# Optimization experiments

Hardware: AMD Instinct MI355X
Metric: run time of the kernel (lower is better)

Reference implementation:

```python
import jax, jax.numpy as jnp
import numpy as np

N_NODES = 50000


def _gcn_norm(edge_index, num_nodes):
    """Add self-loops and compute symmetric GCN normalization per edge.
    Returns (src, dst, norm) with src/dst of length E + N."""
    loop = jnp.arange(num_nodes, dtype=edge_index.dtype)
    src = jnp.concatenate([edge_index[0], loop])
    dst = jnp.concatenate([edge_index[1], loop])
    ones = jnp.ones(dst.shape[0], dtype=jnp.float32)
    deg = jax.ops.segment_sum(ones, dst, num_segments=num_nodes)
    dinv = jnp.where(deg > 0, jax.lax.rsqrt(deg), 0.0)
    norm = dinv[src] * dinv[dst]  # [E + N]
    return src, dst, norm


def _gcn_conv(x, src, dst, norm, W, b, num_nodes):
    h = x @ W                                # [N, out]
    msg = h[src] * norm[:, None]             # gather + scale, [E+N, out]
    out = jax.ops.segment_sum(msg, dst, num_segments=num_nodes)  # scatter-add
    return out + b


def setup_inputs() -> dict:
    key = jax.random.key(0)
    ks = jax.random.split(key, 10)
    F, H = 128, 128
    x = jax.random.normal(ks[0], (N_NODES, F), dtype=jnp.float32)
    edge_index = jax.random.randint(ks[1], (2, 800000), 0, N_NODES, dtype=jnp.int64)
    def glorot(k, fan_in, fan_out):
        s = (6.0 / (fan_in + fan_out)) ** 0.5
        return jax.random.uniform(k, (fan_in, fan_out), jnp.float32, -s, s)
    return {
        "x": x,
        "edge_index": edge_index,
        "W1": glorot(ks[2], F, H), "b1": jnp.zeros((H,), jnp.float32),
        "W2": glorot(ks[3], H, H), "b2": jnp.zeros((H,), jnp.float32),
        "W3": glorot(ks[4], H, H), "b3": jnp.zeros((H,), jnp.float32),
        "W4": glorot(ks[5], H, F), "b4": jnp.zeros((F,), jnp.float32),
    }


def reference(x, edge_index, W1, b1, W2, b2, W3, b3, W4, b4):
    n = x.shape[0]
    src, dst, norm = _gcn_norm(edge_index, n)  # same edges for all 4 layers
    h = jax.nn.relu(_gcn_conv(x, src, dst, norm, W1, b1, n))
    h = jax.nn.relu(_gcn_conv(h, src, dst, norm, W2, b2, n))
    h = jax.nn.relu(_gcn_conv(h, src, dst, norm, W3, b3, n))
    h = jax.nn.relu(_gcn_conv(h, src, dst, norm, W4, b4, n))
    return h
```

## Files before the change

### kernel.cpp

```cpp
#include <hip/hip_runtime.h>
#include <hip/hip_fp16.h>

typedef __attribute__((ext_vector_type(8))) _Float16 half8;
typedef __attribute__((ext_vector_type(4))) float f32x4;

static __device__ __forceinline__ half8 as_half8(uint4 u) {
    union { uint4 u; half8 h; } c; c.u = u; return c.h;
}


__global__ void prep_k(int* __restrict__ cnt, const float* __restrict__ x,
                       __half* __restrict__ Xh, int N) {
    int stride = gridDim.x * 256;
    int tid = blockIdx.x * 256 + threadIdx.x;
    for (int i = tid; i < 12544; i += stride) ((int4*)cnt)[i] = make_int4(0, 0, 0, 0);
    int nOut = N * 16;
    const float4* x4 = (const float4*)x;
    uint4* o4 = (uint4*)Xh;
    for (int i = tid; i < nOut; i += stride) {
        float4 f0 = x4[i * 2 + 0];
        float4 f1 = x4[i * 2 + 1];
        __half2 h0 = __floats2half2_rn(f0.x, f0.y);
        __half2 h1 = __floats2half2_rn(f0.z, f0.w);
        __half2 h2 = __floats2half2_rn(f1.x, f1.y);
        __half2 h3 = __floats2half2_rn(f1.z, f1.w);
        uint4 o;
        o.x = *(unsigned int*)&h0;
        o.y = *(unsigned int*)&h1;
        o.z = *(unsigned int*)&h2;
        o.w = *(unsigned int*)&h3;
        o4[i] = o;
    }
}

__global__ void hist_rank_k(const int* __restrict__ dst, int* __restrict__ cnt,
                            int* __restrict__ rank, int E) {
    int e4 = blockIdx.x * 256 + threadIdx.x;
    int nE4 = E >> 2;
    if (e4 < nE4) {
        int4 d = ((const int4*)dst)[e4];
        int4 r;
        r.x = atomicAdd(&cnt[d.x], 1);
        r.y = atomicAdd(&cnt[d.y], 1);
        r.z = atomicAdd(&cnt[d.z], 1);
        r.w = atomicAdd(&cnt[d.w], 1);
        ((int4*)rank)[e4] = r;
    } else if (e4 == nE4) {
        for (int e = nE4 * 4; e < E; ++e) rank[e] = atomicAdd(&cnt[dst[e]], 1);
    }
}

__global__ void bsum_k(const int* __restrict__ cnt, int* __restrict__ bsum,
                       float* __restrict__ dinv, int n) {
    int b = blockIdx.x, tid = threadIdx.x;
    int base = b * 1024 + tid * 4;
    int4 v = make_int4(0, 0, 0, 0);
    if (base + 3 < n) v = *(const int4*)(cnt + base);
    else {
        if (base + 0 < n) v.x = cnt[base + 0];
        if (base + 1 < n) v.y = cnt[base + 1];
        if (base + 2 < n) v.z = cnt[base + 2];
    }
    if (base + 3 < n) {
        float4 dv;
        dv.x = rsqrtf((float)v.x + 1.0f);
        dv.y = rsqrtf((float)v.y + 1.0f);
        dv.z = rsqrtf((float)v.z + 1.0f);
        dv.w = rsqrtf((float)v.w + 1.0f);
        *(float4*)(dinv + base) = dv;
    } else {
        if (base + 0 < n) dinv[base + 0] = rsqrtf((float)v.x + 1.0f);
        if (base + 1 < n) dinv[base + 1] = rsqrtf((float)v.y + 1.0f);
        if (base + 2 < n) dinv[base + 2] = rsqrtf((float)v.z + 1.0f);
    }
    int s = v.x + v.y + v.z + v.w;
#pragma unroll
    for (int off = 32; off; off >>= 1) s += __shfl_xor(s, off, 64);
    __shared__ int wsh[4];
    if ((tid & 63) == 0) wsh[tid >> 6] = s;
    __syncthreads();
    if (tid == 0) bsum[b] = wsh[0] + wsh[1] + wsh[2] + wsh[3];
}

__global__ void bscan_k(const int* __restrict__ bsum, int* __restrict__ boffs, int nb) {
    int tid = threadIdx.x;
    int lane = tid & 63, wid = tid >> 6;
    int s = (tid < nb) ? bsum[tid] : 0;
    int incl = s;
#pragma unroll
    for (int off = 1; off < 64; off <<= 1) {
        int t = __shfl_up(incl, off, 64);
        if (lane >= off) incl += t;
    }
    __shared__ int wsh[4];
    if (lane == 63) wsh[wid] = incl;
    __syncthreads();
    int woff = 0;
    for (int w = 0; w < wid; ++w) woff += wsh[w];
    if (tid < nb) boffs[tid] = woff + incl - s;
}

__global__ void rowscan_k(const int* __restrict__ cnt, const int* __restrict__ boffs,
                          int* __restrict__ rowptr, int n) {
    int b = blockIdx.x, tid = threadIdx.x;
    int lane = tid & 63, wid = tid >> 6;
    int base = b * 1024 + tid * 4;
    int4 v = make_int4(0, 0, 0, 0);
    if (base + 3 < n) v = *(const int4*)(cnt + base);
    else {
        if (base + 0 < n) v.x = cnt[base + 0];
        if (base + 1 < n) v.y = cnt[base + 1];
        if (base + 2 < n) v.z = cnt[base + 2];
    }
    int s = v.x + v.y + v.z + v.w;
    int incl = s;
#pragma unroll
    for (int off = 1; off < 64; off <<= 1) {
        int t = __shfl_up(incl, off, 64);
        if (lane >= off) incl += t;
    }
    __shared__ int wsh[4];
    if (lane == 63) wsh[wid] = incl;
    __syncthreads();
    int woff = boffs[b];
    for (int w = 0; w < wid; ++w) woff += wsh[w];
    int e0 = woff + incl - s;
    int o0 = e0 + v.x, o1 = o0 + v.y, o2 = o1 + v.z, o3 = o2 + v.w;
    if (base + 0 < n) rowptr[base + 1] = o0;
    if (base + 1 < n) rowptr[base + 2] = o1;
    if (base + 2 < n) rowptr[base + 3] = o2;
    if (base + 3 < n) rowptr[base + 4] = o3;
    if (b == 0 && tid == 0) rowptr[0] = 0;
}

__global__ void pospay_k(const int* __restrict__ src, const int* __restrict__ dst,
                         const int* __restrict__ rank, const int* __restrict__ rowptr,
                         const float* __restrict__ dinv,
                         int* __restrict__ pos, unsigned int* __restrict__ payload, int E) {
    int e4 = blockIdx.x * 256 + threadIdx.x;
    int nE4 = E >> 2;
    if (e4 < nE4) {
        int4 d = ((const int4*)dst)[e4];
        int4 s = ((const int4*)src)[e4];
        int4 r = ((const int4*)rank)[e4];
        int ds[4] = {d.x, d.y, d.z, d.w};
        int ss[4] = {s.x, s.y, s.z, s.w};
        int rs[4] = {r.x, r.y, r.z, r.w};
        int4 po;
        uint4 py;
        int* pop = &po.x;
        unsigned int* pyp = &py.x;
#pragma unroll
        for (int j = 0; j < 4; ++j) {
            pop[j] = rowptr[ds[j]] + rs[j];
            float w = dinv[ss[j]] * dinv[ds[j]];
            unsigned short wh = __half_as_ushort(__float2half(w));
            pyp[j] = ((unsigned int)ss[j] << 16) | (unsigned int)wh;
        }
        ((int4*)pos)[e4] = po;
        ((uint4*)payload)[e4] = py;
    } else if (e4 == nE4) {
        for (int e = nE4 * 4; e < E; ++e) {
            int d = dst[e], s = src[e];
            pos[e] = rowptr[d] + rank[e];
            float w = dinv[s] * dinv[d];
            unsigned short wh = __half_as_ushort(__float2half(w));
            payload[e] = ((unsigned int)s << 16) | (unsigned int)wh;
        }
    }
}

__global__ void scatter8_k(const int* __restrict__ pos, const unsigned int* __restrict__ payload,
                           unsigned int* __restrict__ edata, int E, int S) {
    int stripe = blockIdx.x & 7;
    int lo = stripe * S;
    int hi = min(E, lo + S);
    int e4 = (blockIdx.x >> 3) * 256 + threadIdx.x;
    int nE4 = E >> 2;
    if (e4 < nE4) {
        int4 p = ((const int4*)pos)[e4];
        uint4 y = ((const uint4*)payload)[e4];
        if (p.x >= lo && p.x < hi) edata[p.x] = y.x;
        if (p.y >= lo && p.y < hi) edata[p.y] = y.y;
        if (p.z >= lo && p.z < hi) edata[p.z] = y.z;
        if (p.w >= lo && p.w < hi) edata[p.w] = y.w;
    } else if (e4 == nE4) {
        for (int e = nE4 * 4; e < E; ++e) {
            int p = pos[e];
            if (p >= lo && p < hi) edata[p] = payload[e];
        }
    }
}

__global__ void wshuf_k(const float* __restrict__ W0, const float* __restrict__ W1,
                        const float* __restrict__ W2, const float* __restrict__ W3,
                        uint4* __restrict__ Wshuf) {
    int gid = blockIdx.x * 256 + threadIdx.x;
    int layer = gid >> 11;
    int tid2 = gid & 2047;
    int ks = tid2 >> 9;
    int rem = tid2 & 511;
    int ct = rem >> 6;
    int lane = rem & 63;
    const float* W = (layer == 0) ? W0 : (layer == 1) ? W1 : (layer == 2) ? W2 : W3;
    int col = ct * 16 + (lane & 15);
    int k0 = ks * 32 + (lane >> 4) * 8;
    __half h[8];
#pragma unroll
    for (int j = 0; j < 8; ++j) h[j] = __float2half(W[(k0 + j) * 128 + col]);
    uint4 o;
    o.x = *(unsigned int*)&h[0];
    o.y = *(unsigned int*)&h[2];
    o.z = *(unsigned int*)&h[4];
    o.w = *(unsigned int*)&h[6];
    Wshuf[gid] = o;
}


__global__ __launch_bounds__(256) void gemm_k(const __half* __restrict__ Xh,
                                              const uint4* __restrict__ Wsh,
                                              __half* __restrict__ Hh, int N) {
    __shared__ uint4 bsh[2048];
    int tid = threadIdx.x;
#pragma unroll
    for (int i = 0; i < 8; ++i) bsh[i * 256 + tid] = Wsh[i * 256 + tid];
    __syncthreads();

    int lane = tid & 63;
    int wv = tid >> 6;
    int rbase = blockIdx.x * 256 + wv * 64;
    int lr = lane & 15;
    int lk = lane >> 4;

    const uint4* X4 = (const uint4*)Xh;

    f32x4 acc[4][8];
#pragma unroll
    for (int rt = 0; rt < 4; ++rt)
#pragma unroll
        for (int ct = 0; ct < 8; ++ct) acc[rt][ct] = (f32x4){0.f, 0.f, 0.f, 0.f};

#pragma unroll
    for (int ks = 0; ks < 4; ++ks) {
        half8 a[4];
#pragma unroll
        for (int rt = 0; rt < 4; ++rt) {
            int row = rbase + rt * 16 + lr;
            uint4 u = (row < N) ? X4[(size_t)row * 16 + ks * 4 + lk]
                                : make_uint4(0, 0, 0, 0);
            a[rt] = as_half8(u);
        }
#pragma unroll
        for (int ct = 0; ct < 8; ++ct) {
            half8 b = as_half8(bsh[(ks * 8 + ct) * 64 + lane]);
#pragma unroll
            for (int rt = 0; rt < 4; ++rt) {
                acc[rt][ct] = __builtin_amdgcn_mfma_f32_16x16x32_f16(a[rt], b, acc[rt][ct], 0, 0, 0);
            }
        }
    }

#pragma unroll
    for (int rt = 0; rt < 4; ++rt) {
        int row0 = rbase + rt * 16 + lk * 4;
#pragma unroll
        for (int ct = 0; ct < 8; ++ct) {
            int col = ct * 16 + lr;
            f32x4 v = acc[rt][ct];
#pragma unroll
            for (int r = 0; r < 4; ++r) {
                int row = row0 + r;
                if (row < N) Hh[(size_t)row * 128 + col] = __float2half(v[r]);
            }
        }
    }
}

__device__ __forceinline__ void acc8(float* a, uint4 v, float w) {
    unsigned int u[4] = {v.x, v.y, v.z, v.w};
#pragma unroll
    for (int j = 0; j < 4; ++j) {
        __half2 h = *(__half2*)&u[j];
        float2 f = __half22float2(h);
        a[2 * j + 0] = fmaf(f.x, w, a[2 * j + 0]);
        a[2 * j + 1] = fmaf(f.y, w, a[2 * j + 1]);
    }
}

template <bool F16OUT>
__global__ __launch_bounds__(256) void gather_agg_k(
        const __half* __restrict__ Hh, const int* __restrict__ rowptr,
        const unsigned int* __restrict__ edata, const float* __restrict__ dinv,
        const float* __restrict__ b, void* __restrict__ out, int N) {
    int t = blockIdx.x * 256 + threadIdx.x;
    int i = t >> 4;
    if (i >= N) return;
    int lane = t & 15;
    const uint4* H4 = (const uint4*)Hh;

    float dn = dinv[i];
    float sn = dn * dn;

    float a[8] = {};
    acc8(a, H4[(size_t)i * 16 + lane], sn);

    int p0 = rowptr[i];
    int p1 = rowptr[i + 1];
    int p = p0;
    for (; p + 8 <= p1; p += 8) {
        unsigned int e0 = edata[p + 0];
        unsigned int e1 = edata[p + 1];
        unsigned int e2 = edata[p + 2];
        unsigned int e3 = edata[p + 3];
        unsigned int e4 = edata[p + 4];
        unsigned int e5 = edata[p + 5];
        unsigned int e6 = edata[p + 6];
        unsigned int e7 = edata[p + 7];
        uint4 v0 = H4[(size_t)(e0 >> 16) * 16 + lane];
        uint4 v1 = H4[(size_t)(e1 >> 16) * 16 + lane];
        uint4 v2 = H4[(size_t)(e2 >> 16) * 16 + lane];
        uint4 v3 = H4[(size_t)(e3 >> 16) * 16 + lane];
        uint4 v4 = H4[(size_t)(e4 >> 16) * 16 + lane];
        uint4 v5 = H4[(size_t)(e5 >> 16) * 16 + lane];
        uint4 v6 = H4[(size_t)(e6 >> 16) * 16 + lane];
        uint4 v7 = H4[(size_t)(e7 >> 16) * 16 + lane];
        acc8(a, v0, __half2float(__ushort_as_half((unsigned short)(e0 & 0xffffu))));
        acc8(a, v1, __half2float(__ushort_as_half((unsigned short)(e1 & 0xffffu))));
        acc8(a, v2, __half2float(__ushort_as_half((unsigned short)(e2 & 0xffffu))));
        acc8(a, v3, __half2float(__ushort_as_half((unsigned short)(e3 & 0xffffu))));
        acc8(a, v4, __half2float(__ushort_as_half((unsigned short)(e4 & 0xffffu))));
        acc8(a, v5, __half2float(__ushort_as_half((unsigned short)(e5 & 0xffffu))));
        acc8(a, v6, __half2float(__ushort_as_half((unsigned short)(e6 & 0xffffu))));
        acc8(a, v7, __half2float(__ushort_as_half((unsigned short)(e7 & 0xffffu))));
    }
    for (; p + 4 <= p1; p += 4) {
        unsigned int e0 = edata[p + 0];
        unsigned int e1 = edata[p + 1];
        unsigned int e2 = edata[p + 2];
        unsigned int e3 = edata[p + 3];
        uint4 v0 = H4[(size_t)(e0 >> 16) * 16 + lane];
        uint4 v1 = H4[(size_t)(e1 >> 16) * 16 + lane];
        uint4 v2 = H4[(size_t)(e2 >> 16) * 16 + lane];
        uint4 v3 = H4[(size_t)(e3 >> 16) * 16 + lane];
        acc8(a, v0, __half2float(__ushort_as_half((unsigned short)(e0 & 0xffffu))));
        acc8(a, v1, __half2float(__ushort_as_half((unsigned short)(e1 & 0xffffu))));
        acc8(a, v2, __half2float(__ushort_as_half((unsigned short)(e2 & 0xffffu))));
        acc8(a, v3, __half2float(__ushort_as_half((unsigned short)(e3 & 0xffffu))));
    }
    for (; p < p1; ++p) {
        unsigned int e = edata[p];
        uint4 v = H4[(size_t)(e >> 16) * 16 + lane];
        acc8(a, v, __half2float(__ushort_as_half((unsigned short)(e & 0xffffu))));
    }

    const float4* b4 = (const float4*)b;
    float4 bb0 = b4[lane * 2 + 0];
    float4 bb1 = b4[lane * 2 + 1];
    float r[8];
    r[0] = fmaxf(a[0] + bb0.x, 0.f);
    r[1] = fmaxf(a[1] + bb0.y, 0.f);
    r[2] = fmaxf(a[2] + bb0.z, 0.f);
    r[3] = fmaxf(a[3] + bb0.w, 0.f);
    r[4] = fmaxf(a[4] + bb1.x, 0.f);
    r[5] = fmaxf(a[5] + bb1.y, 0.f);
    r[6] = fmaxf(a[6] + bb1.z, 0.f);
    r[7] = fmaxf(a[7] + bb1.w, 0.f);

    if (F16OUT) {
        __half2 h0 = __floats2half2_rn(r[0], r[1]);
        __half2 h1 = __floats2half2_rn(r[2], r[3]);
        __half2 h2 = __floats2half2_rn(r[4], r[5]);
        __half2 h3 = __floats2half2_rn(r[6], r[7]);
        uint4 o;
        o.x = *(unsigned int*)&h0;
        o.y = *(unsigned int*)&h1;
        o.z = *(unsigned int*)&h2;
        o.w = *(unsigned int*)&h3;
        ((uint4*)out)[(size_t)i * 16 + lane] = o;
    } else {
        float4* orow = (float4*)((float*)out + (size_t)i * 128);
        orow[lane * 2 + 0] = make_float4(r[0], r[1], r[2], r[3]);
        orow[lane * 2 + 1] = make_float4(r[4], r[5], r[6], r[7]);
    }
}


extern "C" void kernel_launch(void* const* d_in, const int* in_sizes, int n_in,
                              void* d_out, int out_size, void* d_ws, size_t ws_size,
                              hipStream_t stream) {
    const float* x = (const float*)d_in[0];
    const int* ei = (const int*)d_in[1];
    const int E = in_sizes[1] / 2;
    const int* srcI = ei;
    const int* dstI = ei + E;
    const float* b[4] = {(const float*)d_in[3], (const float*)d_in[5],
                         (const float*)d_in[7], (const float*)d_in[9]};
    const int N = in_sizes[0] / 128;
    const int Ea = (E + 3) & ~3;

    int* iws = (int*)d_ws;
    int* cnt = iws;
    int* rowptr = iws + 50176;
    float* dinv = (float*)(iws + 100352);
    int* bsum = iws + 150528;
    int* boffs = iws + 150592;
    int* rank = iws + 150656;
    int* pos = rank + Ea;
    unsigned int* payload = (unsigned int*)(pos + Ea);
    unsigned int* edata = payload + Ea;
    uint4* Wshuf = (uint4*)(edata + Ea);
    int* wsEnd = (int*)(Wshuf + 8192);
    __half* Xh = (__half*)wsEnd;
    __half* Hh = (__half*)(wsEnd + (size_t)N * 64);

    dim3 blk(256);
    int gE4 = ((E >> 2) + 1 + 255) / 256;
    int NB = (N + 1023) / 1024;
    int gGemm = (N + 255) / 256;
    int gGather = (N * 16 + 255) / 256;
    int S = (((E + 7) / 8) + 31) & ~31;

    prep_k<<<1024, blk, 0, stream>>>(cnt, x, Xh, N);
    hist_rank_k<<<gE4, blk, 0, stream>>>(dstI, cnt, rank, E);
    bsum_k<<<NB, blk, 0, stream>>>(cnt, bsum, dinv, N);
    bscan_k<<<1, blk, 0, stream>>>(bsum, boffs, NB);
    rowscan_k<<<NB, blk, 0, stream>>>(cnt, boffs, rowptr, N);
    pospay_k<<<gE4, blk, 0, stream>>>(srcI, dstI, rank, rowptr, dinv, pos, payload, E);
    scatter8_k<<<gE4 * 8, blk, 0, stream>>>(pos, payload, edata, E, S);
    wshuf_k<<<32, blk, 0, stream>>>((const float*)d_in[2], (const float*)d_in[4],
                                    (const float*)d_in[6], (const float*)d_in[8], Wshuf);

    const __half* in = Xh;
    for (int l = 0; l < 4; ++l) {
        gemm_k<<<gGemm, blk, 0, stream>>>(in, Wshuf + l * 2048, Hh, N);
        if (l == 3) {
            gather_agg_k<false><<<gGather, blk, 0, stream>>>(Hh, rowptr, edata, dinv, b[l], d_out, N);
        } else {
            gather_agg_k<true><<<gGather, blk, 0, stream>>>(Hh, rowptr, edata, dinv, b[l], Xh, N);
            in = Xh;
        }
    }
}
```

Baseline: 258.1 us.

## Fuse fp32 input conversion into first GEMM, drop block-scan kernel, split gather by feature halves

```diff
diff --git a/kernel.cpp b/kernel.cpp
--- a/kernel.cpp
+++ b/kernel.cpp
@@ -9,28 +9,9 @@
 }
 
 
-__global__ void prep_k(int* __restrict__ cnt, const float* __restrict__ x,
-                       __half* __restrict__ Xh, int N) {
-    int stride = gridDim.x * 256;
-    int tid = blockIdx.x * 256 + threadIdx.x;
-    for (int i = tid; i < 12544; i += stride) ((int4*)cnt)[i] = make_int4(0, 0, 0, 0);
-    int nOut = N * 16;
-    const float4* x4 = (const float4*)x;
-    uint4* o4 = (uint4*)Xh;
-    for (int i = tid; i < nOut; i += stride) {
-        float4 f0 = x4[i * 2 + 0];
-        float4 f1 = x4[i * 2 + 1];
-        __half2 h0 = __floats2half2_rn(f0.x, f0.y);
-        __half2 h1 = __floats2half2_rn(f0.z, f0.w);
-        __half2 h2 = __floats2half2_rn(f1.x, f1.y);
-        __half2 h3 = __floats2half2_rn(f1.z, f1.w);
-        uint4 o;
-        o.x = *(unsigned int*)&h0;
-        o.y = *(unsigned int*)&h1;
-        o.z = *(unsigned int*)&h2;
-        o.w = *(unsigned int*)&h3;
-        o4[i] = o;
-    }
+__global__ void zero_k(int* __restrict__ cnt) {
+    int i = blockIdx.x * 256 + threadIdx.x;
+    if (i < 12544) ((int4*)cnt)[i] = make_int4(0, 0, 0, 0);
 }
 
 __global__ void hist_rank_k(const int* __restrict__ dst, int* __restrict__ cnt,
@@ -82,25 +63,7 @@
     if (tid == 0) bsum[b] = wsh[0] + wsh[1] + wsh[2] + wsh[3];
 }
 
-__global__ void bscan_k(const int* __restrict__ bsum, int* __restrict__ boffs, int nb) {
-    int tid = threadIdx.x;
-    int lane = tid & 63, wid = tid >> 6;
-    int s = (tid < nb) ? bsum[tid] : 0;
-    int incl = s;
-#pragma unroll
-    for (int off = 1; off < 64; off <<= 1) {
-        int t = __shfl_up(incl, off, 64);
-        if (lane >= off) incl += t;
-    }
-    __shared__ int wsh[4];
-    if (lane == 63) wsh[wid] = incl;
-    __syncthreads();
-    int woff = 0;
-    for (int w = 0; w < wid; ++w) woff += wsh[w];
-    if (tid < nb) boffs[tid] = woff + incl - s;
-}
-
-__global__ void rowscan_k(const int* __restrict__ cnt, const int* __restrict__ boffs,
+__global__ void rowscan_k(const int* __restrict__ cnt, const int* __restrict__ bsum,
                           int* __restrict__ rowptr, int n) {
     int b = blockIdx.x, tid = threadIdx.x;
     int lane = tid & 63, wid = tid >> 6;
@@ -122,7 +85,8 @@
     __shared__ int wsh[4];
     if (lane == 63) wsh[wid] = incl;
     __syncthreads();
-    int woff = boffs[b];
+    int woff = 0;
+    for (int w = 0; w < b; ++w) woff += bsum[w];
     for (int w = 0; w < wid; ++w) woff += wsh[w];
     int e0 = woff + incl - s;
     int o0 = e0 + v.x, o1 = o0 + v.y, o2 = o1 + v.z, o3 = o2 + v.w;
@@ -217,7 +181,8 @@
 }
 
 
-__global__ __launch_bounds__(256) void gemm_k(const __half* __restrict__ Xh,
+template <bool F32IN>
+__global__ __launch_bounds__(256) void gemm_k(const void* __restrict__ Xin,
                                               const uint4* __restrict__ Wsh,
                                               __half* __restrict__ Hh, int N) {
     __shared__ uint4 bsh[2048];
@@ -232,8 +197,6 @@
     int lr = lane & 15;
     int lk = lane >> 4;
 
-    const uint4* X4 = (const uint4*)Xh;
-
     f32x4 acc[4][8];
 #pragma unroll
     for (int rt = 0; rt < 4; ++rt)
@@ -246,9 +209,24 @@
 #pragma unroll
         for (int rt = 0; rt < 4; ++rt) {
             int row = rbase + rt * 16 + lr;
-            uint4 u = (row < N) ? X4[(size_t)row * 16 + ks * 4 + lk]
-                                : make_uint4(0, 0, 0, 0);
-            a[rt] = as_half8(u);
+            if (F32IN) {
+                half8 h = (half8)(_Float16)0;
+                if (row < N) {
+                    const float4* xf = (const float4*)((const float*)Xin +
+                                        (size_t)row * 128 + (ks * 4 + lk) * 8);
+                    float4 f0 = xf[0];
+                    float4 f1 = xf[1];
+                    h[0] = (_Float16)f0.x; h[1] = (_Float16)f0.y;
+                    h[2] = (_Float16)f0.z; h[3] = (_Float16)f0.w;
+                    h[4] = (_Float16)f1.x; h[5] = (_Float16)f1.y;
+                    h[6] = (_Float16)f1.z; h[7] = (_Float16)f1.w;
+                }
+                a[rt] = h;
+            } else {
+                uint4 u = (row < N) ? ((const uint4*)Xin)[(size_t)row * 16 + ks * 4 + lk]
+                                    : make_uint4(0, 0, 0, 0);
+                a[rt] = as_half8(u);
+            }
         }
 #pragma unroll
         for (int ct = 0; ct < 8; ++ct) {
@@ -276,33 +254,37 @@
     }
 }
 
-__device__ __forceinline__ void acc8(float* a, uint4 v, float w) {
-    unsigned int u[4] = {v.x, v.y, v.z, v.w};
-#pragma unroll
-    for (int j = 0; j < 4; ++j) {
-        __half2 h = *(__half2*)&u[j];
-        float2 f = __half22float2(h);
-        a[2 * j + 0] = fmaf(f.x, w, a[2 * j + 0]);
-        a[2 * j + 1] = fmaf(f.y, w, a[2 * j + 1]);
-    }
+__device__ __forceinline__ void acc4(float* a, uint2 v, float w) {
+    __half2 h0 = *(__half2*)&v.x;
+    __half2 h1 = *(__half2*)&v.y;
+    float2 f0 = __half22float2(h0);
+    float2 f1 = __half22float2(h1);
+    a[0] = fmaf(f0.x, w, a[0]);
+    a[1] = fmaf(f0.y, w, a[1]);
+    a[2] = fmaf(f1.x, w, a[2]);
+    a[3] = fmaf(f1.y, w, a[3]);
 }
 
 template <bool F16OUT>
 __global__ __launch_bounds__(256) void gather_agg_k(
         const __half* __restrict__ Hh, const int* __restrict__ rowptr,
         const unsigned int* __restrict__ edata, const float* __restrict__ dinv,
-        const float* __restrict__ b, void* __restrict__ out, int N) {
-    int t = blockIdx.x * 256 + threadIdx.x;
+        const float* __restrict__ b, void* __restrict__ out, int N, int G) {
+    int bid = blockIdx.x;
+    int c = (bid >= G) ? 1 : 0;
+    int g = bid - c * G;
+    int t = g * 256 + threadIdx.x;
     int i = t >> 4;
     if (i >= N) return;
     int lane = t & 15;
-    const uint4* H4 = (const uint4*)Hh;
+    int fo = c * 16 + lane;
+    const uint2* H2 = (const uint2*)Hh;
 
     float dn = dinv[i];
     float sn = dn * dn;
 
-    float a[8] = {};
-    acc8(a, H4[(size_t)i * 16 + lane], sn);
+    float a[4] = {};
+    acc4(a, H2[(size_t)i * 32 + fo], sn);
 
     int p0 = rowptr[i];
     int p1 = rowptr[i + 1];
@@ -316,71 +298,59 @@
         unsigned int e5 = edata[p + 5];
         unsigned int e6 = edata[p + 6];
         unsigned int e7 = edata[p + 7];
-        uint4 v0 = H4[(size_t)(e0 >> 16) * 16 + lane];
-        uint4 v1 = H4[(size_t)(e1 >> 16) * 16 + lane];
-        uint4 v2 = H4[(size_t)(e2 >> 16) * 16 + lane];
-        uint4 v3 = H4[(size_t)(e3 >> 16) * 16 + lane];
-        uint4 v4 = H4[(size_t)(e4 >> 16) * 16 + lane];
-        uint4 v5 = H4[(size_t)(e5 >> 16) * 16 + lane];
-        uint4 v6 = H4[(size_t)(e6 >> 16) * 16 + lane];
-        uint4 v7 = H4[(size_t)(e7 >> 16) * 16 + lane];
-        acc8(a, v0, __half2float(__ushort_as_half((unsigned short)(e0 & 0xffffu))));
-        acc8(a, v1, __half2float(__ushort_as_half((unsigned short)(e1 & 0xffffu))));
-        acc8(a, v2, __half2float(__ushort_as_half((unsigned short)(e2 & 0xffffu))));
-        acc8(a, v3, __half2float(__ushort_as_half((unsigned short)(e3 & 0xffffu))));
-        acc8(a, v4, __half2float(__ushort_as_half((unsigned short)(e4 & 0xffffu))));
-        acc8(a, v5, __half2float(__ushort_as_half((unsigned short)(e5 & 0xffffu))));
-        acc8(a, v6, __half2float(__ushort_as_half((unsigned short)(e6 & 0xffffu))));
-        acc8(a, v7, __half2float(__ushort_as_half((unsigned short)(e7 & 0xffffu))));
+        uint2 v0 = H2[(size_t)(e0 >> 16) * 32 + fo];
+        uint2 v1 = H2[(size_t)(e1 >> 16) * 32 + fo];
+        uint2 v2 = H2[(size_t)(e2 >> 16) * 32 + fo];
+        uint2 v3 = H2[(size_t)(e3 >> 16) * 32 + fo];
+        uint2 v4 = H2[(size_t)(e4 >> 16) * 32 + fo];
+        uint2 v5 = H2[(size_t)(e5 >> 16) * 32 + fo];
+        uint2 v6 = H2[(size_t)(e6 >> 16) * 32 + fo];
+        uint2 v7 = H2[(size_t)(e7 >> 16) * 32 + fo];
+        acc4(a, v0, __half2float(__ushort_as_half((unsigned short)(e0 & 0xffffu))));
+        acc4(a, v1, __half2float(__ushort_as_half((unsigned short)(e1 & 0xffffu))));
+        acc4(a, v2, __half2float(__ushort_as_half((unsigned short)(e2 & 0xffffu))));
+        acc4(a, v3, __half2float(__ushort_as_half((unsigned short)(e3 & 0xffffu))));
+        acc4(a, v4, __half2float(__ushort_as_half((unsigned short)(e4 & 0xffffu))));
+        acc4(a, v5, __half2float(__ushort_as_half((unsigned short)(e5 & 0xffffu))));
+        acc4(a, v6, __half2float(__ushort_as_half((unsigned short)(e6 & 0xffffu))));
+        acc4(a, v7, __half2float(__ushort_as_half((unsigned short)(e7 & 0xffffu))));
     }
     for (; p + 4 <= p1; p += 4) {
         unsigned int e0 = edata[p + 0];
         unsigned int e1 = edata[p + 1];
         unsigned int e2 = edata[p + 2];
         unsigned int e3 = edata[p + 3];
-        uint4 v0 = H4[(size_t)(e0 >> 16) * 16 + lane];
-        uint4 v1 = H4[(size_t)(e1 >> 16) * 16 + lane];
-        uint4 v2 = H4[(size_t)(e2 >> 16) * 16 + lane];
-        uint4 v3 = H4[(size_t)(e3 >> 16) * 16 + lane];
-        acc8(a, v0, __half2float(__ushort_as_half((unsigned short)(e0 & 0xffffu))));
-        acc8(a, v1, __half2float(__ushort_as_half((unsigned short)(e1 & 0xffffu))));
-        acc8(a, v2, __half2float(__ushort_as_half((unsigned short)(e2 & 0xffffu))));
-        acc8(a, v3, __half2float(__ushort_as_half((unsigned short)(e3 & 0xffffu))));
+        uint2 v0 = H2[(size_t)(e0 >> 16) * 32 + fo];
+        uint2 v1 = H2[(size_t)(e1 >> 16) * 32 + fo];
+        uint2 v2 = H2[(size_t)(e2 >> 16) * 32 + fo];
+        uint2 v3 = H2[(size_t)(e3 >> 16) * 32 + fo];
+        acc4(a, v0, __half2float(__ushort_as_half((unsigned short)(e0 & 0xffffu))));
+        acc4(a, v1, __half2float(__ushort_as_half((unsigned short)(e1 & 0xffffu))));
+        acc4(a, v2, __half2float(__ushort_as_half((unsigned short)(e2 & 0xffffu))));
+        acc4(a, v3, __half2float(__ushort_as_half((unsigned short)(e3 & 0xffffu))));
     }
     for (; p < p1; ++p) {
         unsigned int e = edata[p];
-        uint4 v = H4[(size_t)(e >> 16) * 16 + lane];
-        acc8(a, v, __half2float(__ushort_as_half((unsigned short)(e & 0xffffu))));
-    }
-
-    const float4* b4 = (const float4*)b;
-    float4 bb0 = b4[lane * 2 + 0];
-    float4 bb1 = b4[lane * 2 + 1];
-    float r[8];
-    r[0] = fmaxf(a[0] + bb0.x, 0.f);
-    r[1] = fmaxf(a[1] + bb0.y, 0.f);
-    r[2] = fmaxf(a[2] + bb0.z, 0.f);
-    r[3] = fmaxf(a[3] + bb0.w, 0.f);
-    r[4] = fmaxf(a[4] + bb1.x, 0.f);
-    r[5] = fmaxf(a[5] + bb1.y, 0.f);
-    r[6] = fmaxf(a[6] + bb1.z, 0.f);
-    r[7] = fmaxf(a[7] + bb1.w, 0.f);
+        uint2 v = H2[(size_t)(e >> 16) * 32 + fo];
+        acc4(a, v, __half2float(__ushort_as_half((unsigned short)(e & 0xffffu))));
+    }
+
+    float4 bb = ((const float4*)b)[fo >> 1 << 1 | (lane & 1)];
+    bb = ((const float4*)b)[fo];
+    float r0 = fmaxf(a[0] + bb.x, 0.f);
+    float r1 = fmaxf(a[1] + bb.y, 0.f);
+    float r2 = fmaxf(a[2] + bb.z, 0.f);
+    float r3 = fmaxf(a[3] + bb.w, 0.f);
 
     if (F16OUT) {
-        __half2 h0 = __floats2half2_rn(r[0], r[1]);
-        __half2 h1 = __floats2half2_rn(r[2], r[3]);
-        __half2 h2 = __floats2half2_rn(r[4], r[5]);
-        __half2 h3 = __floats2half2_rn(r[6], r[7]);
-        uint4 o;
+        __half2 h0 = __floats2half2_rn(r0, r1);
+        __half2 h1 = __floats2half2_rn(r2, r3);
+        uint2 o;
         o.x = *(unsigned int*)&h0;
         o.y = *(unsigned int*)&h1;
-        o.z = *(unsigned int*)&h2;
-        o.w = *(unsigned int*)&h3;
-        ((uint4*)out)[(size_t)i * 16 + lane] = o;
+        ((uint2*)out)[(size_t)i * 32 + fo] = o;
     } else {
-        float4* orow = (float4*)((float*)out + (size_t)i * 128);
-        orow[lane * 2 + 0] = make_float4(r[0], r[1], r[2], r[3]);
-        orow[lane * 2 + 1] = make_float4(r[4], r[5], r[6], r[7]);
+        *(float4*)((float*)out + (size_t)i * 128 + fo * 4) = make_float4(r0, r1, r2, r3);
     }
 }
 
@@ -403,7 +373,6 @@
     int* rowptr = iws + 50176;
     float* dinv = (float*)(iws + 100352);
     int* bsum = iws + 150528;
-    int* boffs = iws + 150592;
     int* rank = iws + 150656;
     int* pos = rank + Ea;
     unsigned int* payload = (unsigned int*)(pos + Ea);
@@ -417,27 +386,25 @@
     int gE4 = ((E >> 2) + 1 + 255) / 256;
     int NB = (N + 1023) / 1024;
     int gGemm = (N + 255) / 256;
-    int gGather = (N * 16 + 255) / 256;
+    int G = (N * 16 + 255) / 256;
     int S = (((E + 7) / 8) + 31) & ~31;
 
-    prep_k<<<1024, blk, 0, stream>>>(cnt, x, Xh, N);
+    zero_k<<<49, blk, 0, stream>>>(cnt);
     hist_rank_k<<<gE4, blk, 0, stream>>>(dstI, cnt, rank, E);
     bsum_k<<<NB, blk, 0, stream>>>(cnt, bsum, dinv, N);
-    bscan_k<<<1, blk, 0, stream>>>(bsum, boffs, NB);
-    rowscan_k<<<NB, blk, 0, stream>>>(cnt, boffs, rowptr, N);
+    rowscan_k<<<NB, blk, 0, stream>>>(cnt, bsum, rowptr, N);
     pospay_k<<<gE4, blk, 0, stream>>>(srcI, dstI, rank, rowptr, dinv, pos, payload, E);
     scatter8_k<<<gE4 * 8, blk, 0, stream>>>(pos, payload, edata, E, S);
     wshuf_k<<<32, blk, 0, stream>>>((const float*)d_in[2], (const float*)d_in[4],
                                     (const float*)d_in[6], (const float*)d_in[8], Wshuf);
 
-    const __half* in = Xh;
     for (int l = 0; l < 4; ++l) {
-        gemm_k<<<gGemm, blk, 0, stream>>>(in, Wshuf + l * 2048, Hh, N);
+        if (l == 0) gemm_k<true><<<gGemm, blk, 0, stream>>>(x, Wshuf, Hh, N);
+        else        gemm_k<false><<<gGemm, blk, 0, stream>>>(Xh, Wshuf + l * 2048, Hh, N);
         if (l == 3) {
-            gather_agg_k<false><<<gGather, blk, 0, stream>>>(Hh, rowptr, edata, dinv, b[l], d_out, N);
+            gather_agg_k<false><<<2 * G, blk, 0, stream>>>(Hh, rowptr, edata, dinv, b[l], d_out, N, G);
         } else {
-            gather_agg_k<true><<<gGather, blk, 0, stream>>>(Hh, rowptr, edata, dinv, b[l], Xh, N);
-            in = Xh;
-        }
-    }
-}
+            gather_agg_k<true><<<2 * G, blk, 0, stream>>>(Hh, rowptr, edata, dinv, b[l], Xh, N, G);
+        }
+    }
+}
```

Result: faster. 251.7 us (-2.5%).
